# Kernel optimization log

Hardware: AMD Instinct MI355X
Metric: run time of the kernel (lower is better)

## Reference

```python
import jax, jax.numpy as jnp
import numpy as np

B = 32768
D = 1024          # input_dim
SEL = 512         # select_dim (per-expert selected features)
E = 6             # num_experts
K = 3             # top_k
SH = 32           # shared_dim
INNER = 64        # cross-attn inner dim (4 heads * 16)
HID = 128         # expert hidden


def setup_inputs() -> dict:
    key = jax.random.key(0)
    ks = jax.random.split(key, 16)
    s = lambda i, shape, scale=0.02: (jax.random.normal(ks[i], shape, jnp.float32) * scale)
    return {
        "x": jax.random.normal(ks[0], (B, D), jnp.float32),
        # CrossAttention(query_dim=512, context_dim=512, heads=4, dim_head=16)
        "Wq": s(1, (512, INNER)),
        "Wk": s(2, (512, INNER)),
        "Wv": s(3, (512, INNER)),
        "Wo": s(4, (INNER, 512)),
        "bo": jnp.zeros((512,), jnp.float32),
        # shared_proj: Linear(512, 32)
        "Wsp": s(5, (512, SH)),
        "bsp": jnp.zeros((SH,), jnp.float32),
        # gate: Linear(1024, 6)
        "Wg": s(6, (D, E)),
        "bg": jnp.zeros((E,), jnp.float32),
        # per-expert feature-mask logits
        "mask_logits": jax.random.normal(ks[7], (E, D), jnp.float32),
        # expert MLPs: Linear(544,128) -> ReLU -> Linear(128,1), stacked over experts
        "W1": s(8, (E, SEL + SH, HID)),
        "b1": jnp.zeros((E, HID), jnp.float32),
        "W2": s(9, (E, HID, 1)),
        "b2": jnp.zeros((E, 1), jnp.float32),
    }


def _moe_forward(x, Wq, Wk, Wv, Wo, bo, Wsp, bsp, Wg, bg, mask_logits, W1, b1, W2, b2):
    x_sem = x[:, :512]
    x_vis = x[:, 512:]

    # CrossAttention with a single query token attending to a single context
    # token: softmax over one key is identically 1, so attn output == v.
    v = x_vis @ Wv                      # [B, INNER]
    shared_token = v @ Wo + bo          # to_out Linear, [B, 512]
    shared_info = shared_token @ Wsp + bsp  # [B, SH]

    # Gating: top-k experts per sample, softmax over selected logits
    gate_logits = x @ Wg + bg                       # [B, E]
    topk_scores, topk_idx = jax.lax.top_k(gate_logits, K)  # [B, K]
    topk_w = jax.nn.softmax(topk_scores, axis=1)    # [B, K]

    # Per-expert learned feature selection (top-512 of sigmoid(mask_logits));
    # sigmoid is monotonic but kept for faithfulness.
    mask_prob = jax.nn.sigmoid(mask_logits)         # [E, D]
    _, sel_idx = jax.lax.top_k(mask_prob, SEL)      # [E, SEL]

    # Dense expert evaluation (every expert on every sample), then gather the
    # routed outputs -- same math as the original scatter loop.
    x_sel = jnp.take(x, sel_idx, axis=1)            # [B, E, SEL]
    h = jnp.einsum('bes,esh->beh', x_sel, W1[:, :SEL, :])
    h = h + jnp.einsum('bd,edh->beh', shared_info, W1[:, SEL:, :])
    h = jax.nn.relu(h + b1[None])                   # [B, E, HID]
    expert_out = jnp.einsum('beh,eh->be', h, W2[:, :, 0]) + b2[None, :, 0]  # [B, E]

    routed = jnp.take_along_axis(expert_out, topk_idx, axis=1)  # [B, K]
    return jnp.sum(topk_w * routed, axis=1, keepdims=True)      # [B, 1]


def reference(x, Wq, Wk, Wv, Wo, bo, Wsp, bsp, Wg, bg, mask_logits, W1, b1, W2, b2):
    return _moe_forward(x, Wq, Wk, Wv, Wo, bo, Wsp, bsp, Wg, bg, mask_logits, W1, b1, W2, b2)
```

## Files before the change

### kernel.cpp

```cpp
#include <hip/hip_runtime.h>

#define B 32768
#define D 1024
#define SEL 512
#define E 6
#define K 3
#define SH 32
#define HID 128
#define NKT 16

typedef __attribute__((ext_vector_type(8))) short bf16x8;
typedef __attribute__((ext_vector_type(4))) float f32x4;

__device__ __forceinline__ unsigned short f2bf(float f) {
  unsigned u = __float_as_uint(f);
  return (unsigned short)((u + 0x7fffu + ((u >> 16) & 1u)) >> 16);
}

__device__ __forceinline__ void gload_lds16(const void* g, void* l) {
  __builtin_amdgcn_global_load_lds(
      (const __attribute__((address_space(1))) void*)g,
      (__attribute__((address_space(3))) void*)l, 16, 0, 0);
}

__global__ void k_sel(const float* __restrict__ ml, int* __restrict__ inv,
                      int* __restrict__ cnt) {
  __shared__ float row[D];
  const int e = blockIdx.x, t = threadIdx.x;
  if (t == 0) cnt[e] = 0;
  row[t] = ml[e * D + t];
  __syncthreads();
  const float v = row[t];
  int rank = 0;
  for (int i = 0; i < D; ++i) {
    float u = row[i];
    rank += (u > v) || (u == v && i < t);
  }
  inv[e * D + t] = (rank < SEL) ? rank : -1;
}

__global__ __launch_bounds__(256) void k_wowsp(
    const float* __restrict__ Wo, const float* __restrict__ Wsp,
    const float* __restrict__ bo, const float* __restrict__ bsp,
    float* __restrict__ WoWsp, float* __restrict__ bfull) {
  __shared__ float red[256];
  const int t = threadIdx.x;
  const int j = t & 31, chunk = t >> 5;
  const int blk = blockIdx.x;
  float p = 0.f;
  if (blk < 64) {
    const int i = blk;
    for (int c = chunk * 64; c < chunk * 64 + 64; ++c)
      p += Wo[i * 512 + c] * Wsp[c * SH + j];
    red[t] = p;
    __syncthreads();
    if (t < 32) {
      float s = 0.f;
      #pragma unroll
      for (int k = 0; k < 8; ++k) s += red[k * 32 + j];
      WoWsp[i * SH + j] = s;
    }
  } else {
    for (int c = chunk * 64; c < chunk * 64 + 64; ++c)
      p += bo[c] * Wsp[c * SH + j];
    red[t] = p;
    __syncthreads();
    if (t < 32) {
      float s = bsp[j];
      #pragma unroll
      for (int k = 0; k < 8; ++k) s += red[k * 32 + j];
      bfull[j] = s;
    }
  }
}

__global__ __launch_bounds__(256) void k_wfull2(
    const float* __restrict__ Wv, const float* __restrict__ WoWsp,
    float* __restrict__ Wfull) {
  __shared__ float wsh[64 * SH];
  const int t = threadIdx.x;
  for (int idx = t; idx < 64 * SH; idx += 256) wsh[idx] = WoWsp[idx];
  __syncthreads();
  const int c = blockIdx.x * 8 + (t >> 5), j = t & 31;
  float p = 0.f;
  #pragma unroll 8
  for (int i = 0; i < 64; ++i) p += Wv[c * 64 + i] * wsh[i * SH + j];
  Wfull[c * SH + j] = p;
}

__global__ __launch_bounds__(256) void k_w1c(
    const float* __restrict__ W1, const float* __restrict__ b1,
    const int* __restrict__ inv, const float* __restrict__ Wfull,
    const float* __restrict__ bfull,
    unsigned short* __restrict__ W1eT, float* __restrict__ b1c) {
  __shared__ float w1b[SH];
  __shared__ float bf[SH];
  const int e = blockIdx.x >> 7, h = blockIdx.x & 127;
  const int t = threadIdx.x;
  const float* We = W1 + (size_t)e * (SEL + SH) * HID;
  if (t < SH) { w1b[t] = We[(size_t)(SEL + t) * HID + h]; bf[t] = bfull[t]; }
  __syncthreads();
  const int* iv = inv + e * D;
  unsigned short* dst = W1eT + ((size_t)e * HID + h) * D;
  #pragma unroll
  for (int it = 0; it < 4; ++it) {
    int d = t + it * 256;
    int s = iv[d];
    float v = (s >= 0) ? We[(size_t)s * HID + h] : 0.f;
    if (d >= 512) {
      const float* wf = Wfull + (size_t)(d - 512) * SH;
      float p = 0.f;
      #pragma unroll
      for (int j = 0; j < SH; ++j) p += wf[j] * w1b[j];
      v += p;
    }
    dst[d] = f2bf(v);
  }
  if (t == 0) {
    float p = b1[e * HID + h];
    for (int j = 0; j < SH; ++j) p += bf[j] * w1b[j];
    b1c[e * HID + h] = p;
  }
}

template<bool WRITE_XBF>
__global__ __launch_bounds__(256) void k_xbf_gate(
    const float* __restrict__ x, const float* __restrict__ Wg,
    const float* __restrict__ bg, unsigned short* __restrict__ xbf,
    float* __restrict__ gl) {
  const int w = threadIdx.x >> 6, lane = threadIdx.x & 63;
  const int wid = blockIdx.x * 4 + w;
  float wg[4][4][E];
  #pragma unroll
  for (int i = 0; i < 4; ++i)
    #pragma unroll
    for (int q = 0; q < 4; ++q) {
      const float* wr = Wg + (size_t)(i * 256 + lane * 4 + q) * E;
      #pragma unroll
      for (int e2 = 0; e2 < E; ++e2) wg[i][q][e2] = wr[e2];
    }
  for (int tok = wid * 4; tok < wid * 4 + 4; ++tok) {
    const float4* xp = (const float4*)(x + (size_t)tok * D);
    float acc[E] = {};
    #pragma unroll
    for (int i = 0; i < 4; ++i) {
      float4 v = xp[i * 64 + lane];
      if (WRITE_XBF) {
        ushort4 h4;
        h4.x = f2bf(v.x); h4.y = f2bf(v.y); h4.z = f2bf(v.z); h4.w = f2bf(v.w);
        *(ushort4*)((char*)xbf + (size_t)tok * 2048 + i * 512 + lane * 8) = h4;
      }
      #pragma unroll
      for (int q = 0; q < 4; ++q) {
        float xv = (&v.x)[q];
        #pragma unroll
        for (int e2 = 0; e2 < E; ++e2) acc[e2] += xv * wg[i][q][e2];
      }
    }
    #pragma unroll
    for (int e2 = 0; e2 < E; ++e2) {
      float s = acc[e2];
      s += __shfl_xor(s, 1); s += __shfl_xor(s, 2); s += __shfl_xor(s, 4);
      s += __shfl_xor(s, 8); s += __shfl_xor(s, 16); s += __shfl_xor(s, 32);
      acc[e2] = s;
    }
    if (lane == 0) {
      #pragma unroll
      for (int e2 = 0; e2 < E; ++e2) gl[(size_t)tok * E + e2] = acc[e2] + bg[e2];
    }
  }
}

__global__ __launch_bounds__(256) void k_topk(
    const float* __restrict__ gl, int* __restrict__ cnt,
    int* __restrict__ clist, float* __restrict__ wlist) {
  const int tok = blockIdx.x * 256 + threadIdx.x;
  const int lane = threadIdx.x & 63;
  float gv[E];
  #pragma unroll
  for (int e2 = 0; e2 < E; ++e2) gv[e2] = gl[(size_t)tok * E + e2];
  int idx[K]; float sc[K];
  bool used[E] = {};
  #pragma unroll
  for (int k = 0; k < K; ++k) {
    float best = -1e30f; int bi = 0;
    for (int e2 = 0; e2 < E; ++e2)
      if (!used[e2] && gv[e2] > best) { best = gv[e2]; bi = e2; }
    used[bi] = true; sc[k] = best; idx[k] = bi;
  }
  float s1 = __expf(sc[1] - sc[0]), s2 = __expf(sc[2] - sc[0]);
  float inv_s = 1.f / (1.f + s1 + s2);
  float tw[K] = {inv_s, s1 * inv_s, s2 * inv_s};
  const unsigned long long below = (1ULL << lane) - 1ULL;
  #pragma unroll
  for (int e2 = 0; e2 < E; ++e2) {
    int myk = -1;
    #pragma unroll
    for (int k = 0; k < K; ++k) if (idx[k] == e2) myk = k;
    unsigned long long m = __ballot(myk >= 0);
    if (m) {
      int tot = __popcll(m);
      int leader = __ffsll((long long)m) - 1;
      int base = 0;
      if (lane == leader) base = atomicAdd(&cnt[e2], tot);
      base = __shfl(base, leader);
      if (myk >= 0) {
        int pos = base + __popcll(m & below);
        clist[e2 * B + pos] = (tok << 2) | myk;
        wlist[e2 * B + pos] = tw[myk];
      }
    }
  }
}

template<int AMODE>
__global__ __launch_bounds__(256) void k_gemm(
    const float* __restrict__ x, const unsigned short* __restrict__ xbf,
    const unsigned short* __restrict__ W1eT,
    const int* __restrict__ cnt, const int* __restrict__ clist,
    const float* __restrict__ wlist,
    const float* __restrict__ b1c, const float* __restrict__ W2,
    const float* __restrict__ b2, float* __restrict__ eo4) {
  __shared__ __align__(16) char ldsA[128 * 128];
  __shared__ __align__(16) char ldsB[128 * 128];
  __shared__ int tokl[128];
  __shared__ float red[128];

  const int t = threadIdx.x;
  const int e = blockIdx.x >> 8;
  const int bm = blockIdx.x & 255;
  const int n = cnt[e];
  if (bm * 128 >= n) return;
  const int cb = e * B;

  if (t < 128) {
    int gr = bm * 128 + t;
    tokl[t] = clist[cb + (gr < n ? gr : 0)] >> 2;
  }
  __syncthreads();

  const int w = t >> 6, lane = t & 63;
  const int g = lane >> 4, j = lane & 15;
  const int swz = ((lane & 7) * 16) ^ ((lane >> 3) << 4);

  const char* srcB[4];
  #pragma unroll
  for (int q = 0; q < 4; ++q)
    srcB[q] = (const char*)W1eT +
              (size_t)(e * HID + w * 32 + q * 8 + (lane >> 3)) * (D * 2) + swz;
  const char* srcA[4];
  if (AMODE == 0) {
    #pragma unroll
    for (int q = 0; q < 4; ++q)
      srcA[q] = (const char*)xbf +
                (size_t)tokl[w * 32 + q * 8 + (lane >> 3)] * 2048 + swz;
  }

  f32x4 acc[2][8] = {};

  for (int kt = 0; kt < NKT; ++kt) {
    if (kt) __syncthreads();
    if (AMODE == 0) {
      #pragma unroll
      for (int q = 0; q < 4; ++q)
        gload_lds16(srcA[q] + kt * 128, ldsA + w * 4096 + q * 1024);
    }
    #pragma unroll
    for (int q = 0; q < 4; ++q)
      gload_lds16(srcB[q] + kt * 128, ldsB + w * 4096 + q * 1024);
    if (AMODE == 1) {
      #pragma unroll
      for (int it = 0; it < 8; ++it) {
        int r = (t >> 4) + it * 16;
        const float4 v =
            *(const float4*)(x + (size_t)tokl[r] * D + kt * 64 + (t & 15) * 4);
        ushort4 h4;
        h4.x = f2bf(v.x); h4.y = f2bf(v.y); h4.z = f2bf(v.z); h4.w = f2bf(v.w);
        *(ushort4*)(ldsA + r * 128 + (((t & 15) * 8) ^ ((r & 7) << 4))) = h4;
      }
    }
    __syncthreads();
    #pragma unroll
    for (int kk = 0; kk < 2; ++kk) {
      const int kb = kk * 64 + g * 16;
      bf16x8 aF[2];
      #pragma unroll
      for (int fm = 0; fm < 2; ++fm) {
        int row = w * 32 + fm * 16 + j;
        aF[fm] = *(const bf16x8*)(ldsA + row * 128 + (kb ^ ((row & 7) << 4)));
      }
      #pragma unroll
      for (int fn = 0; fn < 8; ++fn) {
        int col = fn * 16 + j;
        bf16x8 bF = *(const bf16x8*)(ldsB + col * 128 + (kb ^ ((col & 7) << 4)));
        acc[0][fn] = __builtin_amdgcn_mfma_f32_16x16x32_bf16(aF[0], bF, acc[0][fn], 0, 0, 0);
        acc[1][fn] = __builtin_amdgcn_mfma_f32_16x16x32_bf16(aF[1], bF, acc[1][fn], 0, 0, 0);
      }
    }
  }

  float vb1[8], vw2[8];
  #pragma unroll
  for (int fn = 0; fn < 8; ++fn) {
    int col = fn * 16 + j;
    vb1[fn] = b1c[e * HID + col];
    vw2[fn] = W2[e * HID + col];
  }
  #pragma unroll
  for (int fm = 0; fm < 2; ++fm) {
    #pragma unroll
    for (int r = 0; r < 4; ++r) {
      float s = 0.f;
      #pragma unroll
      for (int fn = 0; fn < 8; ++fn)
        s += fmaxf(acc[fm][fn][r] + vb1[fn], 0.f) * vw2[fn];
      s += __shfl_xor(s, 1); s += __shfl_xor(s, 2);
      s += __shfl_xor(s, 4); s += __shfl_xor(s, 8);
      if (j == 0) red[w * 32 + fm * 16 + g * 4 + r] = s;
    }
  }
  __syncthreads();
  if (t < 128) {
    int gr = bm * 128 + t;
    if (gr < n) {
      int en = clist[cb + gr];
      eo4[(size_t)(en >> 2) * 4 + (en & 3)] = wlist[cb + gr] * (red[t] + b2[e]);
    }
  }
}

__global__ void k_comb2(const float* __restrict__ eo4, float* __restrict__ out) {
  const int tok = blockIdx.x * 256 + threadIdx.x;
  float4 v = *(const float4*)(eo4 + (size_t)tok * 4);
  out[tok] = v.x + v.y + v.z;
}

extern "C" void kernel_launch(void* const* d_in, const int* in_sizes, int n_in,
                              void* d_out, int out_size, void* d_ws, size_t ws_size,
                              hipStream_t stream) {
  const float* x   = (const float*)d_in[0];
  const float* Wv  = (const float*)d_in[3];
  const float* Wo  = (const float*)d_in[4];
  const float* bo  = (const float*)d_in[5];
  const float* Wsp = (const float*)d_in[6];
  const float* bsp = (const float*)d_in[7];
  const float* Wg  = (const float*)d_in[8];
  const float* bg  = (const float*)d_in[9];
  const float* ml  = (const float*)d_in[10];
  const float* W1  = (const float*)d_in[11];
  const float* b1  = (const float*)d_in[12];
  const float* W2  = (const float*)d_in[13];
  const float* b2  = (const float*)d_in[14];
  float* out = (float*)d_out;

  char* ws = (char*)d_ws;
  int*   inv   = (int*)ws;
  float* WoWsp = (float*)(ws + 32768);
  float* Wfull = (float*)(ws + 49152);
  float* bfull = (float*)(ws + 114688);
  float* b1c   = (float*)(ws + 118784);
  int*   cnt   = (int*)(ws + 126976);
  float* gl    = (float*)(ws + 131072);
  int*   clist = (int*)(ws + 917504);
  float* wlist = (float*)(ws + 1703936);
  float* eo4   = (float*)(ws + 2490368);
  unsigned short* W1eT = (unsigned short*)(ws + 3014656);
  unsigned short* xbf  = (unsigned short*)(ws + 4587520);
  const bool use_xbf = ws_size >= (size_t)4587520 + (size_t)B * D * 2;

  k_sel<<<E, D, 0, stream>>>(ml, inv, cnt);
  k_wowsp<<<65, 256, 0, stream>>>(Wo, Wsp, bo, bsp, WoWsp, bfull);
  k_wfull2<<<64, 256, 0, stream>>>(Wv, WoWsp, Wfull);
  k_w1c<<<E * HID, 256, 0, stream>>>(W1, b1, inv, Wfull, bfull, W1eT, b1c);
  if (use_xbf)
    k_xbf_gate<true><<<B / 16, 256, 0, stream>>>(x, Wg, bg, xbf, gl);
  else
    k_xbf_gate<false><<<B / 16, 256, 0, stream>>>(x, Wg, bg, xbf, gl);
  k_topk<<<B / 256, 256, 0, stream>>>(gl, cnt, clist, wlist);
  if (use_xbf)
    k_gemm<0><<<E * 256, 256, 0, stream>>>(x, xbf, W1eT, cnt, clist, wlist, b1c, W2, b2, eo4);
  else
    k_gemm<1><<<E * 256, 256, 0, stream>>>(x, xbf, W1eT, cnt, clist, wlist, b1c, W2, b2, eo4);
  k_comb2<<<B / 256, 256, 0, stream>>>(eo4, out);
}
```

Measured before the change: 197.9 us.

## Fuse gate projection with top-k routing using LDS-tiled token blocks

Replaces the per-wave gate kernel and the separate top-k kernel with one kernel in which each block stages 64 tokens of x and the whole Wg in LDS. Each wave computes partial logits over a slice of the features, the partials are reduced through LDS, and wave 0 does the top-k, softmax and atomic list building directly. This removes the gate-logit buffer round trip and one launch, and replaces the cross-lane shuffle reductions with per-thread accumulation. In exchange it uses a large LDS footprint (about 54 KB), which limits occupancy, and the block syncs twice for each of the 16 feature chunks.

```diff
diff --git a/kernel.cpp b/kernel.cpp
--- a/kernel.cpp
+++ b/kernel.cpp
@@ -124,90 +124,104 @@
 }
 
 template<bool WRITE_XBF>
-__global__ __launch_bounds__(256) void k_xbf_gate(
+__global__ __launch_bounds__(256) void k_gate2(
     const float* __restrict__ x, const float* __restrict__ Wg,
     const float* __restrict__ bg, unsigned short* __restrict__ xbf,
-    float* __restrict__ gl) {
-  const int w = threadIdx.x >> 6, lane = threadIdx.x & 63;
-  const int wid = blockIdx.x * 4 + w;
-  float wg[4][4][E];
-  #pragma unroll
-  for (int i = 0; i < 4; ++i)
+    int* __restrict__ cnt, int* __restrict__ clist, float* __restrict__ wlist) {
+  __shared__ float wgs[D * 8];
+  __shared__ float xs[64 * 65];
+  __shared__ float rbuf[3 * 64 * 6];
+  const int t = threadIdx.x;
+  const int w = t >> 6, l = t & 63;
+  const int tok0 = blockIdx.x * 64;
+
+  for (int i = t; i < D * 6; i += 256) {
+    int d = i / 6, e = i % 6;
+    wgs[d * 8 + e] = Wg[i];
+  }
+  for (int d = t; d < D; d += 256) { wgs[d * 8 + 6] = 0.f; wgs[d * 8 + 7] = 0.f; }
+
+  f32x4 accA = {0.f, 0.f, 0.f, 0.f};
+  f32x4 accB = {0.f, 0.f, 0.f, 0.f};
+
+  for (int c = 0; c < 16; ++c) {
+    __syncthreads();
     #pragma unroll
     for (int q = 0; q < 4; ++q) {
-      const float* wr = Wg + (size_t)(i * 256 + lane * 4 + q) * E;
-      #pragma unroll
-      for (int e2 = 0; e2 < E; ++e2) wg[i][q][e2] = wr[e2];
-    }
-  for (int tok = wid * 4; tok < wid * 4 + 4; ++tok) {
-    const float4* xp = (const float4*)(x + (size_t)tok * D);
-    float acc[E] = {};
-    #pragma unroll
-    for (int i = 0; i < 4; ++i) {
-      float4 v = xp[i * 64 + lane];
+      int fid = t + q * 256;
+      int row = fid >> 4, col = fid & 15;
+      float4 v = *(const float4*)(x + (size_t)(tok0 + row) * D + c * 64 + col * 4);
       if (WRITE_XBF) {
         ushort4 h4;
         h4.x = f2bf(v.x); h4.y = f2bf(v.y); h4.z = f2bf(v.z); h4.w = f2bf(v.w);
-        *(ushort4*)((char*)xbf + (size_t)tok * 2048 + i * 512 + lane * 8) = h4;
-      }
-      #pragma unroll
-      for (int q = 0; q < 4; ++q) {
-        float xv = (&v.x)[q];
-        #pragma unroll
-        for (int e2 = 0; e2 < E; ++e2) acc[e2] += xv * wg[i][q][e2];
-      }
-    }
+        *(ushort4*)(xbf + (size_t)(tok0 + row) * D + c * 64 + col * 4) = h4;
+      }
+      float* dst = &xs[row * 65 + col * 4];
+      dst[0] = v.x; dst[1] = v.y; dst[2] = v.z; dst[3] = v.w;
+    }
+    __syncthreads();
+    const int dbase = c * 64 + w * 16;
+    #pragma unroll
+    for (int dd = 0; dd < 16; ++dd) {
+      const int dg = dbase + dd;
+      f32x4 wa = *(const f32x4*)&wgs[dg * 8];
+      f32x4 wb = *(const f32x4*)&wgs[dg * 8 + 4];
+      float xv = xs[l * 65 + w * 16 + dd];
+      accA += xv * wa;
+      accB += xv * wb;
+    }
+  }
+
+  if (w > 0) {
+    float* rb = &rbuf[((w - 1) * 64 + l) * 6];
+    rb[0] = accA[0]; rb[1] = accA[1]; rb[2] = accA[2]; rb[3] = accA[3];
+    rb[4] = accB[0]; rb[5] = accB[1];
+  }
+  __syncthreads();
+  if (w == 0) {
+    float gv[E];
+    gv[0] = accA[0]; gv[1] = accA[1]; gv[2] = accA[2];
+    gv[3] = accA[3]; gv[4] = accB[0]; gv[5] = accB[1];
+    #pragma unroll
+    for (int p = 0; p < 3; ++p) {
+      const float* rb = &rbuf[(p * 64 + l) * 6];
+      #pragma unroll
+      for (int e2 = 0; e2 < E; ++e2) gv[e2] += rb[e2];
+    }
+    #pragma unroll
+    for (int e2 = 0; e2 < E; ++e2) gv[e2] += bg[e2];
+
+    const int tok = tok0 + l;
+    int idx[K]; float sc[K];
+    bool used[E] = {};
+    #pragma unroll
+    for (int k = 0; k < K; ++k) {
+      float best = -1e30f; int bi = 0;
+      for (int e2 = 0; e2 < E; ++e2)
+        if (!used[e2] && gv[e2] > best) { best = gv[e2]; bi = e2; }
+      used[bi] = true; sc[k] = best; idx[k] = bi;
+    }
+    float s1 = __expf(sc[1] - sc[0]), s2 = __expf(sc[2] - sc[0]);
+    float inv_s = 1.f / (1.f + s1 + s2);
+    float tw[K] = {inv_s, s1 * inv_s, s2 * inv_s};
+    const unsigned long long below = (1ULL << l) - 1ULL;
     #pragma unroll
     for (int e2 = 0; e2 < E; ++e2) {
-      float s = acc[e2];
-      s += __shfl_xor(s, 1); s += __shfl_xor(s, 2); s += __shfl_xor(s, 4);
-      s += __shfl_xor(s, 8); s += __shfl_xor(s, 16); s += __shfl_xor(s, 32);
-      acc[e2] = s;
-    }
-    if (lane == 0) {
-      #pragma unroll
-      for (int e2 = 0; e2 < E; ++e2) gl[(size_t)tok * E + e2] = acc[e2] + bg[e2];
-    }
-  }
-}
-
-__global__ __launch_bounds__(256) void k_topk(
-    const float* __restrict__ gl, int* __restrict__ cnt,
-    int* __restrict__ clist, float* __restrict__ wlist) {
-  const int tok = blockIdx.x * 256 + threadIdx.x;
-  const int lane = threadIdx.x & 63;
-  float gv[E];
-  #pragma unroll
-  for (int e2 = 0; e2 < E; ++e2) gv[e2] = gl[(size_t)tok * E + e2];
-  int idx[K]; float sc[K];
-  bool used[E] = {};
-  #pragma unroll
-  for (int k = 0; k < K; ++k) {
-    float best = -1e30f; int bi = 0;
-    for (int e2 = 0; e2 < E; ++e2)
-      if (!used[e2] && gv[e2] > best) { best = gv[e2]; bi = e2; }
-    used[bi] = true; sc[k] = best; idx[k] = bi;
-  }
-  float s1 = __expf(sc[1] - sc[0]), s2 = __expf(sc[2] - sc[0]);
-  float inv_s = 1.f / (1.f + s1 + s2);
-  float tw[K] = {inv_s, s1 * inv_s, s2 * inv_s};
-  const unsigned long long below = (1ULL << lane) - 1ULL;
-  #pragma unroll
-  for (int e2 = 0; e2 < E; ++e2) {
-    int myk = -1;
-    #pragma unroll
-    for (int k = 0; k < K; ++k) if (idx[k] == e2) myk = k;
-    unsigned long long m = __ballot(myk >= 0);
-    if (m) {
-      int tot = __popcll(m);
-      int leader = __ffsll((long long)m) - 1;
-      int base = 0;
-      if (lane == leader) base = atomicAdd(&cnt[e2], tot);
-      base = __shfl(base, leader);
-      if (myk >= 0) {
-        int pos = base + __popcll(m & below);
-        clist[e2 * B + pos] = (tok << 2) | myk;
-        wlist[e2 * B + pos] = tw[myk];
+      int myk = -1;
+      #pragma unroll
+      for (int k = 0; k < K; ++k) if (idx[k] == e2) myk = k;
+      unsigned long long m = __ballot(myk >= 0);
+      if (m) {
+        int tot = __popcll(m);
+        int leader = __ffsll((long long)m) - 1;
+        int base = 0;
+        if (l == leader) base = atomicAdd(&cnt[e2], tot);
+        base = __shfl(base, leader);
+        if (myk >= 0) {
+          int pos = base + __popcll(m & below);
+          clist[e2 * B + pos] = (tok << 2) | myk;
+          wlist[e2 * B + pos] = tw[myk];
+        }
       }
     }
   }
@@ -355,28 +369,26 @@
 
   char* ws = (char*)d_ws;
   int*   inv   = (int*)ws;
-  float* WoWsp = (float*)(ws + 32768);
-  float* Wfull = (float*)(ws + 49152);
-  float* bfull = (float*)(ws + 114688);
-  float* b1c   = (float*)(ws + 118784);
-  int*   cnt   = (int*)(ws + 126976);
-  float* gl    = (float*)(ws + 131072);
-  int*   clist = (int*)(ws + 917504);
-  float* wlist = (float*)(ws + 1703936);
-  float* eo4   = (float*)(ws + 2490368);
-  unsigned short* W1eT = (unsigned short*)(ws + 3014656);
-  unsigned short* xbf  = (unsigned short*)(ws + 4587520);
-  const bool use_xbf = ws_size >= (size_t)4587520 + (size_t)B * D * 2;
+  float* WoWsp = (float*)(ws + 24576);
+  float* Wfull = (float*)(ws + 32768);
+  float* bfull = (float*)(ws + 98304);
+  float* b1c   = (float*)(ws + 102400);
+  int*   cnt   = (int*)(ws + 106496);
+  int*   clist = (int*)(ws + 925696);
+  float* wlist = (float*)(ws + 1712128);
+  float* eo4   = (float*)(ws + 2498560);
+  unsigned short* W1eT = (unsigned short*)(ws + 3022848);
+  unsigned short* xbf  = (unsigned short*)(ws + 4595712);
+  const bool use_xbf = ws_size >= (size_t)4595712 + (size_t)B * D * 2;
 
   k_sel<<<E, D, 0, stream>>>(ml, inv, cnt);
   k_wowsp<<<65, 256, 0, stream>>>(Wo, Wsp, bo, bsp, WoWsp, bfull);
   k_wfull2<<<64, 256, 0, stream>>>(Wv, WoWsp, Wfull);
   k_w1c<<<E * HID, 256, 0, stream>>>(W1, b1, inv, Wfull, bfull, W1eT, b1c);
   if (use_xbf)
-    k_xbf_gate<true><<<B / 16, 256, 0, stream>>>(x, Wg, bg, xbf, gl);
+    k_gate2<true><<<B / 64, 256, 0, stream>>>(x, Wg, bg, xbf, cnt, clist, wlist);
   else
-    k_xbf_gate<false><<<B / 16, 256, 0, stream>>>(x, Wg, bg, xbf, gl);
-  k_topk<<<B / 256, 256, 0, stream>>>(gl, cnt, clist, wlist);
+    k_gate2<false><<<B / 64, 256, 0, stream>>>(x, Wg, bg, xbf, cnt, clist, wlist);
   if (use_xbf)
     k_gemm<0><<<E * 256, 256, 0, stream>>>(x, xbf, W1eT, cnt, clist, wlist, b1c, W2, b2, eo4);
   else
```

Result: faster. 189.9 us (-4.1%).

## Compute gate logits with split-bf16 MFMA and fuse top-k routing into gate kernel

Applied to the files above, without the earlier changes.

Replaces the scalar FP32 gate dot-product kernel with an MFMA kernel. It splits x and Wg into bf16 hi/lo pairs and does four MFMAs per step to keep near-FP32 accuracy. Tokens whose 3rd and 4th logits are nearly tied are recomputed exactly in FP32 so routing stays faithful. The separate top-k kernel and the gate-logit buffer are folded into the same kernel, removing a launch and a global round-trip, at the cost of more LDS traffic and conversion ALU work.

```diff
diff --git a/kernel.cpp b/kernel.cpp
--- a/kernel.cpp
+++ b/kernel.cpp
@@ -16,6 +16,9 @@
   unsigned u = __float_as_uint(f);
   return (unsigned short)((u + 0x7fffu + ((u >> 16) & 1u)) >> 16);
 }
+__device__ __forceinline__ float bf2f(unsigned short h) {
+  return __uint_as_float((unsigned)h << 16);
+}
 
 __device__ __forceinline__ void gload_lds16(const void* g, void* l) {
   __builtin_amdgcn_global_load_lds(
@@ -42,14 +45,16 @@
 __global__ __launch_bounds__(256) void k_wowsp(
     const float* __restrict__ Wo, const float* __restrict__ Wsp,
     const float* __restrict__ bo, const float* __restrict__ bsp,
-    float* __restrict__ WoWsp, float* __restrict__ bfull) {
+    const float* __restrict__ Wg,
+    float* __restrict__ WoWsp, float* __restrict__ bfull,
+    unsigned short* __restrict__ WgS) {
   __shared__ float red[256];
   const int t = threadIdx.x;
   const int j = t & 31, chunk = t >> 5;
   const int blk = blockIdx.x;
-  float p = 0.f;
   if (blk < 64) {
     const int i = blk;
+    float p = 0.f;
     for (int c = chunk * 64; c < chunk * 64 + 64; ++c)
       p += Wo[i * 512 + c] * Wsp[c * SH + j];
     red[t] = p;
@@ -60,7 +65,8 @@
       for (int k = 0; k < 8; ++k) s += red[k * 32 + j];
       WoWsp[i * SH + j] = s;
     }
-  } else {
+  } else if (blk == 64) {
+    float p = 0.f;
     for (int c = chunk * 64; c < chunk * 64 + 64; ++c)
       p += bo[c] * Wsp[c * SH + j];
     red[t] = p;
@@ -71,6 +77,14 @@
       for (int k = 0; k < 8; ++k) s += red[k * 32 + j];
       bfull[j] = s;
     }
+  } else {
+    const int idx = (blk - 65) * 256 + t;
+    const int col = idx >> 10, k = idx & 1023;
+    float wv = (col < E) ? Wg[(size_t)k * E + col] : 0.f;
+    unsigned short hi = f2bf(wv);
+    unsigned short lo = f2bf(wv - bf2f(hi));
+    WgS[col * D + k] = hi;
+    WgS[16 * D + col * D + k] = lo;
   }
 }
 
@@ -124,90 +138,139 @@
 }
 
 template<bool WRITE_XBF>
-__global__ __launch_bounds__(256) void k_xbf_gate(
-    const float* __restrict__ x, const float* __restrict__ Wg,
-    const float* __restrict__ bg, unsigned short* __restrict__ xbf,
-    float* __restrict__ gl) {
-  const int w = threadIdx.x >> 6, lane = threadIdx.x & 63;
-  const int wid = blockIdx.x * 4 + w;
-  float wg[4][4][E];
-  #pragma unroll
-  for (int i = 0; i < 4; ++i)
-    #pragma unroll
-    for (int q = 0; q < 4; ++q) {
-      const float* wr = Wg + (size_t)(i * 256 + lane * 4 + q) * E;
-      #pragma unroll
-      for (int e2 = 0; e2 < E; ++e2) wg[i][q][e2] = wr[e2];
-    }
-  for (int tok = wid * 4; tok < wid * 4 + 4; ++tok) {
-    const float4* xp = (const float4*)(x + (size_t)tok * D);
-    float acc[E] = {};
-    #pragma unroll
-    for (int i = 0; i < 4; ++i) {
-      float4 v = xp[i * 64 + lane];
-      if (WRITE_XBF) {
-        ushort4 h4;
-        h4.x = f2bf(v.x); h4.y = f2bf(v.y); h4.z = f2bf(v.z); h4.w = f2bf(v.w);
-        *(ushort4*)((char*)xbf + (size_t)tok * 2048 + i * 512 + lane * 8) = h4;
-      }
-      #pragma unroll
-      for (int q = 0; q < 4; ++q) {
-        float xv = (&v.x)[q];
+__global__ __launch_bounds__(256) void k_xgate(
+    const float* __restrict__ x, const unsigned short* __restrict__ WgS,
+    const float* __restrict__ Wg, const float* __restrict__ bg,
+    unsigned short* __restrict__ xbf,
+    int* __restrict__ cnt, int* __restrict__ clist, float* __restrict__ wlist) {
+  __shared__ __align__(16) char ldsAh[64 * 128];
+  __shared__ __align__(16) char ldsAl[64 * 128];
+  __shared__ __align__(16) char ldsW[4096];
+  __shared__ float gl_s[64][8];
+  const int t = threadIdx.x;
+  const int bm = blockIdx.x;
+  const int w = t >> 6, lane = t & 63;
+  const int g = lane >> 4, j = lane & 15;
+  const int swz = ((lane & 7) * 16) ^ ((lane >> 3) << 4);
+
+  const char* srcW = (const char*)WgS +
+                     (size_t)(w * 8 + (lane >> 3)) * (D * 2) + swz;
+
+  f32x4 acc = {0.f, 0.f, 0.f, 0.f};
+
+  for (int kt = 0; kt < NKT; ++kt) {
+    if (kt) __syncthreads();
+    gload_lds16(srcW + kt * 128, ldsW + w * 1024);
+    #pragma unroll
+    for (int it = 0; it < 4; ++it) {
+      int r = (t >> 4) + it * 16;
+      const float4 v =
+          *(const float4*)(x + (size_t)(bm * 64 + r) * D + kt * 64 + (t & 15) * 4);
+      ushort4 hh, ll;
+      hh.x = f2bf(v.x); hh.y = f2bf(v.y); hh.z = f2bf(v.z); hh.w = f2bf(v.w);
+      ll.x = f2bf(v.x - bf2f(hh.x)); ll.y = f2bf(v.y - bf2f(hh.y));
+      ll.z = f2bf(v.z - bf2f(hh.z)); ll.w = f2bf(v.w - bf2f(hh.w));
+      if (WRITE_XBF)
+        *(ushort4*)(xbf + (size_t)(bm * 64 + r) * D + kt * 64 + (t & 15) * 4) = hh;
+      const int ao = r * 128 + (((t & 15) * 8) ^ ((r & 7) << 4));
+      *(ushort4*)(ldsAh + ao) = hh;
+      *(ushort4*)(ldsAl + ao) = ll;
+    }
+    __syncthreads();
+    #pragma unroll
+    for (int kk = 0; kk < 2; ++kk) {
+      const int kb = kk * 64 + g * 16;
+      const int wo = kb ^ ((j & 7) << 4);
+      bf16x8 bh = *(const bf16x8*)(ldsW + j * 128 + wo);
+      bf16x8 bl = *(const bf16x8*)(ldsW + 2048 + j * 128 + wo);
+      const int row = w * 16 + j;
+      const int aoff = row * 128 + (kb ^ ((row & 7) << 4));
+      bf16x8 ah = *(const bf16x8*)(ldsAh + aoff);
+      bf16x8 al = *(const bf16x8*)(ldsAl + aoff);
+      acc = __builtin_amdgcn_mfma_f32_16x16x32_bf16(ah, bh, acc, 0, 0, 0);
+      acc = __builtin_amdgcn_mfma_f32_16x16x32_bf16(ah, bl, acc, 0, 0, 0);
+      acc = __builtin_amdgcn_mfma_f32_16x16x32_bf16(al, bh, acc, 0, 0, 0);
+      acc = __builtin_amdgcn_mfma_f32_16x16x32_bf16(al, bl, acc, 0, 0, 0);
+    }
+  }
+  if (j < E) {
+    #pragma unroll
+    for (int ri = 0; ri < 4; ++ri)
+      gl_s[w * 16 + g * 4 + ri][j] = acc[ri];
+  }
+  __syncthreads();
+  if (t < 64) {
+    const int tok = bm * 64 + t;
+    float gv[E];
+    #pragma unroll
+    for (int e2 = 0; e2 < E; ++e2) gv[e2] = gl_s[t][e2] + bg[e2];
+
+    float s4[4];
+    {
+      bool used[E] = {};
+      #pragma unroll
+      for (int k = 0; k < 4; ++k) {
+        float best = -1e30f; int bi = 0;
+        for (int e2 = 0; e2 < E; ++e2)
+          if (!used[e2] && gv[e2] > best) { best = gv[e2]; bi = e2; }
+        used[bi] = true; s4[k] = best;
+      }
+    }
+    unsigned long long flags = __ballot(s4[2] - s4[3] < 4e-3f);
+    while (flags) {
+      const int fl = __ffsll((long long)flags) - 1;
+      flags &= flags - 1;
+      const int tokf = bm * 64 + fl;
+      float ex[E] = {};
+      for (int i = 0; i < 16; ++i) {
+        const int d = t + 64 * i;
+        float xv = x[(size_t)tokf * D + d];
+        const float* wr = Wg + (size_t)d * E;
         #pragma unroll
-        for (int e2 = 0; e2 < E; ++e2) acc[e2] += xv * wg[i][q][e2];
-      }
-    }
+        for (int e2 = 0; e2 < E; ++e2) ex[e2] += xv * wr[e2];
+      }
+      #pragma unroll
+      for (int e2 = 0; e2 < E; ++e2) {
+        float s = ex[e2];
+        s += __shfl_xor(s, 1); s += __shfl_xor(s, 2); s += __shfl_xor(s, 4);
+        s += __shfl_xor(s, 8); s += __shfl_xor(s, 16); s += __shfl_xor(s, 32);
+        ex[e2] = s;
+      }
+      if (t == fl) {
+        #pragma unroll
+        for (int e2 = 0; e2 < E; ++e2) gv[e2] = ex[e2] + bg[e2];
+      }
+    }
+    int idx[K]; float sc[K];
+    bool used[E] = {};
+    #pragma unroll
+    for (int k = 0; k < K; ++k) {
+      float best = -1e30f; int bi = 0;
+      for (int e2 = 0; e2 < E; ++e2)
+        if (!used[e2] && gv[e2] > best) { best = gv[e2]; bi = e2; }
+      used[bi] = true; sc[k] = best; idx[k] = bi;
+    }
+    float s1 = __expf(sc[1] - sc[0]), s2 = __expf(sc[2] - sc[0]);
+    float inv_s = 1.f / (1.f + s1 + s2);
+    float tw[K] = {inv_s, s1 * inv_s, s2 * inv_s};
+    const unsigned long long below = (1ULL << t) - 1ULL;
     #pragma unroll
     for (int e2 = 0; e2 < E; ++e2) {
-      float s = acc[e2];
-      s += __shfl_xor(s, 1); s += __shfl_xor(s, 2); s += __shfl_xor(s, 4);
-      s += __shfl_xor(s, 8); s += __shfl_xor(s, 16); s += __shfl_xor(s, 32);
-      acc[e2] = s;
-    }
-    if (lane == 0) {
-      #pragma unroll
-      for (int e2 = 0; e2 < E; ++e2) gl[(size_t)tok * E + e2] = acc[e2] + bg[e2];
-    }
-  }
-}
-
-__global__ __launch_bounds__(256) void k_topk(
-    const float* __restrict__ gl, int* __restrict__ cnt,
-    int* __restrict__ clist, float* __restrict__ wlist) {
-  const int tok = blockIdx.x * 256 + threadIdx.x;
-  const int lane = threadIdx.x & 63;
-  float gv[E];
-  #pragma unroll
-  for (int e2 = 0; e2 < E; ++e2) gv[e2] = gl[(size_t)tok * E + e2];
-  int idx[K]; float sc[K];
-  bool used[E] = {};
-  #pragma unroll
-  for (int k = 0; k < K; ++k) {
-    float best = -1e30f; int bi = 0;
-    for (int e2 = 0; e2 < E; ++e2)
-      if (!used[e2] && gv[e2] > best) { best = gv[e2]; bi = e2; }
-    used[bi] = true; sc[k] = best; idx[k] = bi;
-  }
-  float s1 = __expf(sc[1] - sc[0]), s2 = __expf(sc[2] - sc[0]);
-  float inv_s = 1.f / (1.f + s1 + s2);
-  float tw[K] = {inv_s, s1 * inv_s, s2 * inv_s};
-  const unsigned long long below = (1ULL << lane) - 1ULL;
-  #pragma unroll
-  for (int e2 = 0; e2 < E; ++e2) {
-    int myk = -1;
-    #pragma unroll
-    for (int k = 0; k < K; ++k) if (idx[k] == e2) myk = k;
-    unsigned long long m = __ballot(myk >= 0);
-    if (m) {
-      int tot = __popcll(m);
-      int leader = __ffsll((long long)m) - 1;
-      int base = 0;
-      if (lane == leader) base = atomicAdd(&cnt[e2], tot);
-      base = __shfl(base, leader);
-      if (myk >= 0) {
-        int pos = base + __popcll(m & below);
-        clist[e2 * B + pos] = (tok << 2) | myk;
-        wlist[e2 * B + pos] = tw[myk];
+      int myk = -1;
+      #pragma unroll
+      for (int k = 0; k < K; ++k) if (idx[k] == e2) myk = k;
+      unsigned long long m = __ballot(myk >= 0);
+      if (m) {
+        int tot = __popcll(m);
+        int leader = __ffsll((long long)m) - 1;
+        int base = 0;
+        if (t == leader) base = atomicAdd(&cnt[e2], tot);
+        base = __shfl(base, leader);
+        if (myk >= 0) {
+          int pos = base + __popcll(m & below);
+          clist[e2 * B + pos] = (tok << 2) | myk;
+          wlist[e2 * B + pos] = tw[myk];
+        }
       }
     }
   }
@@ -360,23 +423,22 @@
   float* bfull = (float*)(ws + 114688);
   float* b1c   = (float*)(ws + 118784);
   int*   cnt   = (int*)(ws + 126976);
-  float* gl    = (float*)(ws + 131072);
-  int*   clist = (int*)(ws + 917504);
-  float* wlist = (float*)(ws + 1703936);
-  float* eo4   = (float*)(ws + 2490368);
-  unsigned short* W1eT = (unsigned short*)(ws + 3014656);
-  unsigned short* xbf  = (unsigned short*)(ws + 4587520);
-  const bool use_xbf = ws_size >= (size_t)4587520 + (size_t)B * D * 2;
+  unsigned short* WgS = (unsigned short*)(ws + 131072);
+  int*   clist = (int*)(ws + 262144);
+  float* wlist = (float*)(ws + 1048576);
+  float* eo4   = (float*)(ws + 1835008);
+  unsigned short* W1eT = (unsigned short*)(ws + 2359296);
+  unsigned short* xbf  = (unsigned short*)(ws + 3932160);
+  const bool use_xbf = ws_size >= (size_t)3932160 + (size_t)B * D * 2;
 
   k_sel<<<E, D, 0, stream>>>(ml, inv, cnt);
-  k_wowsp<<<65, 256, 0, stream>>>(Wo, Wsp, bo, bsp, WoWsp, bfull);
+  k_wowsp<<<129, 256, 0, stream>>>(Wo, Wsp, bo, bsp, Wg, WoWsp, bfull, WgS);
   k_wfull2<<<64, 256, 0, stream>>>(Wv, WoWsp, Wfull);
   k_w1c<<<E * HID, 256, 0, stream>>>(W1, b1, inv, Wfull, bfull, W1eT, b1c);
   if (use_xbf)
-    k_xbf_gate<true><<<B / 16, 256, 0, stream>>>(x, Wg, bg, xbf, gl);
+    k_xgate<true><<<B / 64, 256, 0, stream>>>(x, WgS, Wg, bg, xbf, cnt, clist, wlist);
   else
-    k_xbf_gate<false><<<B / 16, 256, 0, stream>>>(x, Wg, bg, xbf, gl);
-  k_topk<<<B / 256, 256, 0, stream>>>(gl, cnt, clist, wlist);
+    k_xgate<false><<<B / 64, 256, 0, stream>>>(x, WgS, Wg, bg, xbf, cnt, clist, wlist);
   if (use_xbf)
     k_gemm<0><<<E * 256, 256, 0, stream>>>(x, xbf, W1eT, cnt, clist, wlist, b1c, W2, b2, eo4);
   else
```

Result: faster. 175.7 us (-11.2%).
